# Kernel optimization log

Hardware: AMD Instinct MI355X
Metric: run time of the kernel (lower is better)

## Reference

```python
import jax, jax.numpy as jnp
import numpy as np

EPS = 1e-8  # torch F.cosine_similarity default eps


def _cos_gram(x):
    # row-normalize with eps-clamped norms, then Gram matrix [N, N]
    norms = jnp.maximum(jnp.linalg.norm(x, axis=1, keepdims=True), EPS)
    xn = x / norms
    return xn @ xn.T


def setup_inputs() -> dict:
    key = jax.random.key(0)
    k1, k2 = jax.random.split(key)
    N, D = 8192, 128
    return {
        "feat_q": jax.random.normal(k1, (N, D), dtype=jnp.float32),
        "feat_k": jax.random.normal(k2, (N, D), dtype=jnp.float32),
    }


def reference(feat_q, feat_k):
    feat_k = jax.lax.stop_gradient(feat_k)  # feat_k.detach()
    N = feat_q.shape[0]
    qsim = _cos_gram(feat_q)  # [N, N]
    ksim = _cos_gram(feat_k)  # [N, N]
    # mean of (qsim - ksim)^2 over all off-diagonal (i != j) pairs
    diff2 = (qsim - ksim) ** 2
    off_diag = ~jnp.eye(N, dtype=bool)
    denom = jnp.asarray(N * (N - 1), dtype=diff2.dtype)
    loss = jnp.sum(jnp.where(off_diag, diff2, 0.0)) / denom
    return loss
```

## Files before the change

### kernel.cpp

```cpp
#include <hip/hip_runtime.h>
#include <hip/hip_bf16.h>

#define NROWS 8192
#define DDIM  128
#define KTOT  256
#define GT_ROWB (NROWS * 2)
#define NKCH  32
#define KCH   (NROWS / NKCH)
#define LDSPAD 258

typedef unsigned short ushort_t;
typedef unsigned int   uint_t;
typedef __attribute__((ext_vector_type(8))) short short8;
typedef __attribute__((ext_vector_type(4))) float floatx4;

#define LDS_PTR(p) ((__attribute__((address_space(3))) void*)(p))
#define GLB_PTR(p) ((const __attribute__((address_space(1))) void*)(p))

static __device__ inline ushort_t f2bf(float f) {
    union { float f; uint_t u; } a; a.f = f;
    uint_t u = a.u + 0x7fffu + ((a.u >> 16) & 1u);
    return (ushort_t)(u >> 16);
}

__global__ __launch_bounds__(256) void norm_t_kernel(
    const float* __restrict__ q, const float* __restrict__ k,
    ushort_t* __restrict__ Gt, double* acc)
{
    __shared__ ushort_t lds[64 * LDSPAD];
    if (blockIdx.x == 0 && threadIdx.x == 0) *acc = 0.0;
    int w = threadIdx.x >> 6;
    int l = threadIdx.x & 63;

    #pragma unroll
    for (int i = 0; i < 16; ++i) {
        int rl  = w * 16 + i;
        int row = blockIdx.x * 64 + rl;
        {
            float2 v = ((const float2*)(q + (size_t)row * DDIM))[l];
            float ss = v.x * v.x + v.y * v.y;
            #pragma unroll
            for (int o = 32; o > 0; o >>= 1) ss += __shfl_xor(ss, o, 64);
            float inv = rsqrtf(fmaxf(ss, 1e-16f));
            uint_t p = (uint_t)f2bf(v.x * inv) | ((uint_t)f2bf(v.y * inv) << 16);
            *(uint_t*)&lds[rl * LDSPAD + 2 * l] = p;
        }
        {
            float2 v = ((const float2*)(k + (size_t)row * DDIM))[l];
            float ss = v.x * v.x + v.y * v.y;
            #pragma unroll
            for (int o = 32; o > 0; o >>= 1) ss += __shfl_xor(ss, o, 64);
            float inv = rsqrtf(fmaxf(ss, 1e-16f));
            uint_t p = (uint_t)f2bf(v.x * inv) | ((uint_t)f2bf(v.y * inv) << 16);
            *(uint_t*)&lds[rl * LDSPAD + 128 + 2 * l] = p;
        }
    }
    __syncthreads();

    int a = threadIdx.x;
    char* gdst = (char*)Gt + (size_t)a * GT_ROWB + (size_t)blockIdx.x * 128;
    #pragma unroll
    for (int g = 0; g < 8; ++g) {
        union { ushort_t u16[8]; uint4 v; } tmp;
        #pragma unroll
        for (int e = 0; e < 8; ++e)
            tmp.u16[e] = lds[(g * 8 + e) * LDSPAD + a];
        *(uint4*)(gdst + g * 16) = tmp.v;
    }
}

__global__ __launch_bounds__(128) void gram_a_kernel(
    const ushort_t* __restrict__ Gt, float* __restrict__ P)
{
    __shared__ ushort_t sA[64 * KCH];
    __shared__ ushort_t sB[64 * KCH];

    int tile = blockIdx.x >> 5;
    int c    = blockIdx.x & 31;
    int ti   = tile >> 2, tj = tile & 3;
    int tid  = threadIdx.x;

    const char* gA = (const char*)Gt + (size_t)(ti * 64) * GT_ROWB + c * (KCH * 2);
    const char* gB = (const char*)Gt + (size_t)(tj * 64) * GT_ROWB + c * (KCH * 2);

    #pragma unroll
    for (int it = 0; it < 16; ++it) {
        int chunk = it * 128 + tid;
        int row = chunk >> 5, phys = chunk & 31;
        int logical = phys ^ (row & 7);
        __builtin_amdgcn_global_load_lds(GLB_PTR(gA + (size_t)row * GT_ROWB + logical * 16),
                                         LDS_PTR((char*)sA + chunk * 16), 16, 0, 0);
    }
    #pragma unroll
    for (int it = 0; it < 16; ++it) {
        int chunk = it * 128 + tid;
        int row = chunk >> 5, phys = chunk & 31;
        int logical = phys ^ (row & 7);
        __builtin_amdgcn_global_load_lds(GLB_PTR(gB + (size_t)row * GT_ROWB + logical * 16),
                                         LDS_PTR((char*)sB + chunk * 16), 16, 0, 0);
    }
    __syncthreads();

    int w    = tid >> 6;
    int l    = tid & 63;
    int m    = l & 15;
    int quad = l >> 4;

    floatx4 accC[2][4];
    #pragma unroll
    for (int at = 0; at < 2; ++at)
        #pragma unroll
        for (int bt = 0; bt < 4; ++bt)
            accC[at][bt] = (floatx4){0.f, 0.f, 0.f, 0.f};

    #pragma unroll
    for (int kp = 0; kp < 8; ++kp) {
        short8 af[2], bf[4];
        #pragma unroll
        for (int at = 0; at < 2; ++at) {
            int ra   = w * 32 + at * 16 + m;
            int phys = (kp * 4 + quad) ^ (ra & 7);
            af[at] = *(const short8*)&sA[ra * KCH + phys * 8];
        }
        #pragma unroll
        for (int bt = 0; bt < 4; ++bt) {
            int rb   = bt * 16 + m;
            int phys = (kp * 4 + quad) ^ (rb & 7);
            bf[bt] = *(const short8*)&sB[rb * KCH + phys * 8];
        }
        #pragma unroll
        for (int at = 0; at < 2; ++at)
            #pragma unroll
            for (int bt = 0; bt < 4; ++bt)
                accC[at][bt] = __builtin_amdgcn_mfma_f32_16x16x32_bf16(af[at], bf[bt], accC[at][bt], 0, 0, 0);
    }

    float* pt = P + ((size_t)tile * NKCH + c) * 4096;
    #pragma unroll
    for (int at = 0; at < 2; ++at)
        #pragma unroll
        for (int bt = 0; bt < 4; ++bt)
            #pragma unroll
            for (int r = 0; r < 4; ++r) {
                int row = w * 32 + at * 16 + quad * 4 + r;
                int col = bt * 16 + m;
                pt[row * 64 + col] = accC[at][bt][r];
            }
}

__global__ __launch_bounds__(256) void gram_b_kernel(
    const float* __restrict__ P, double* acc)
{
    __shared__ float wsum[4];
    int e    = blockIdx.x * 256 + threadIdx.x;
    int tile = e >> 12;
    int idx  = e & 4095;

    float s = 0.f;
    #pragma unroll
    for (int c = 0; c < NKCH; ++c)
        s += P[((size_t)tile * NKCH + c) * 4096 + idx];

    int ti = tile >> 2, tj = tile & 3;
    float wgt = ((ti < 2) == (tj < 2)) ? 1.f : -1.f;
    float v = wgt * s * s;

    int w = threadIdx.x >> 6, l = threadIdx.x & 63;
    #pragma unroll
    for (int o = 32; o > 0; o >>= 1) v += __shfl_xor(v, o, 64);
    if (l == 0) wsum[w] = v;
    __syncthreads();
    if (threadIdx.x == 0) {
        double t = (double)wsum[0] + (double)wsum[1] + (double)wsum[2] + (double)wsum[3];
        atomicAdd(acc, t);
    }
}

__global__ void finalize_kernel(const double* acc, float* out) {
    out[0] = (float)(*acc * (1.0 / ((double)NROWS * (double)(NROWS - 1))));
}

extern "C" void kernel_launch(void* const* d_in, const int* in_sizes, int n_in,
                              void* d_out, int out_size, void* d_ws, size_t ws_size,
                              hipStream_t stream) {
    const float* q = (const float*)d_in[0];
    const float* k = (const float*)d_in[1];
    float* out = (float*)d_out;

    double*   acc = (double*)d_ws;
    ushort_t* Gt  = (ushort_t*)((char*)d_ws + 256);
    float*    P   = (float*)((char*)d_ws + 256 + (size_t)KTOT * GT_ROWB);

    norm_t_kernel<<<NROWS / 64, 256, 0, stream>>>(q, k, Gt, acc);
    gram_a_kernel<<<16 * NKCH, 128, 0, stream>>>(Gt, P);
    gram_b_kernel<<<256, 256, 0, stream>>>(P, acc);
    finalize_kernel<<<1, 1, 0, stream>>>(acc, out);
}
```

Baseline: 77.73 us.

## Exploit Gram symmetry, split K finer, vectorize norm loads, fuse finalize

The 256x256 feature Gram over the N dimension is symmetric, so only the 10 upper-triangular 64x64 tile pairs are computed and off-diagonal pairs are weighted by two. The K dimension is split into 64 chunks instead of 32 to raise block count, and gram_a gets a two-block occupancy hint. The normalization kernel uses float4 loads with half-wave row processing and a padded LDS stride. The finalize kernel is removed in favour of a last-block-done atomic counter in gram_b, which saves a launch but adds a fence and an atomic per block.

```diff
diff --git a/kernel.cpp b/kernel.cpp
--- a/kernel.cpp
+++ b/kernel.cpp
@@ -5,9 +5,11 @@
 #define DDIM  128
 #define KTOT  256
 #define GT_ROWB (NROWS * 2)
-#define NKCH  32
-#define KCH   (NROWS / NKCH)
-#define LDSPAD 258
+#define NKCH  64
+#define CHN   (NROWS / NKCH)
+#define NPAIR 10
+#define GB_BLOCKS 160
+#define LDSPAD 260
 
 typedef unsigned short ushort_t;
 typedef unsigned int   uint_t;
@@ -23,36 +25,48 @@
     return (ushort_t)(u >> 16);
 }
 
+static __device__ inline void pair_decode(int p, int* ti, int* tj) {
+    int i = 0, len = 4;
+    while (p >= len) { p -= len; len--; i++; }
+    *ti = i; *tj = i + p;
+}
+
 __global__ __launch_bounds__(256) void norm_t_kernel(
     const float* __restrict__ q, const float* __restrict__ k,
-    ushort_t* __restrict__ Gt, double* acc)
+    ushort_t* __restrict__ Gt, double* acc, uint_t* counter)
 {
     __shared__ ushort_t lds[64 * LDSPAD];
-    if (blockIdx.x == 0 && threadIdx.x == 0) *acc = 0.0;
-    int w = threadIdx.x >> 6;
-    int l = threadIdx.x & 63;
-
-    #pragma unroll
-    for (int i = 0; i < 16; ++i) {
-        int rl  = w * 16 + i;
+    if (blockIdx.x == 0 && threadIdx.x == 0) { *acc = 0.0; *counter = 0u; }
+    int w  = threadIdx.x >> 6;
+    int l  = threadIdx.x & 63;
+    int h  = l >> 5;
+    int li = l & 31;
+
+    #pragma unroll
+    for (int i = 0; i < 8; ++i) {
+        int rl  = w * 16 + 2 * i + h;
         int row = blockIdx.x * 64 + rl;
         {
-            float2 v = ((const float2*)(q + (size_t)row * DDIM))[l];
-            float ss = v.x * v.x + v.y * v.y;
-            #pragma unroll
-            for (int o = 32; o > 0; o >>= 1) ss += __shfl_xor(ss, o, 64);
+            float4 v = ((const float4*)(q + (size_t)row * DDIM))[li];
+            float ss = v.x * v.x + v.y * v.y + v.z * v.z + v.w * v.w;
+            #pragma unroll
+            for (int o = 16; o > 0; o >>= 1) ss += __shfl_xor(ss, o, 64);
             float inv = rsqrtf(fmaxf(ss, 1e-16f));
-            uint_t p = (uint_t)f2bf(v.x * inv) | ((uint_t)f2bf(v.y * inv) << 16);
-            *(uint_t*)&lds[rl * LDSPAD + 2 * l] = p;
+            uint2 p2;
+            p2.x = (uint_t)f2bf(v.x * inv) | ((uint_t)f2bf(v.y * inv) << 16);
+            p2.y = (uint_t)f2bf(v.z * inv) | ((uint_t)f2bf(v.w * inv) << 16);
+            *(uint2*)&lds[rl * LDSPAD + 4 * li] = p2;
         }
         {
-            float2 v = ((const float2*)(k + (size_t)row * DDIM))[l];
-            float ss = v.x * v.x + v.y * v.y;
-            #pragma unroll
-            for (int o = 32; o > 0; o >>= 1) ss += __shfl_xor(ss, o, 64);
+            float4 v = ((const float4*)(k + (size_t)row * DDIM))[li];
+            float ss = v.x * v.x + v.y * v.y + v.z * v.z + v.w * v.w;
+            #pragma unroll
+            for (int o = 16; o > 0; o >>= 1) ss += __shfl_xor(ss, o, 64);
             float inv = rsqrtf(fmaxf(ss, 1e-16f));
-            uint_t p = (uint_t)f2bf(v.x * inv) | ((uint_t)f2bf(v.y * inv) << 16);
-            *(uint_t*)&lds[rl * LDSPAD + 128 + 2 * l] = p;
+            uint2 p2;
+            p2.x = (uint_t)f2bf(v.x * inv) | ((uint_t)f2bf(v.y * inv) << 16);
+            p2.y = (uint_t)f2bf(v.z * inv) | ((uint_t)f2bf(v.w * inv) << 16);
+            *(uint2*)&lds[rl * LDSPAD + 128 + 4 * li] = p2;
         }
     }
     __syncthreads();
@@ -69,35 +83,36 @@
     }
 }
 
-__global__ __launch_bounds__(128) void gram_a_kernel(
+__global__ __launch_bounds__(128, 2) void gram_a_kernel(
     const ushort_t* __restrict__ Gt, float* __restrict__ P)
 {
-    __shared__ ushort_t sA[64 * KCH];
-    __shared__ ushort_t sB[64 * KCH];
-
-    int tile = blockIdx.x >> 5;
-    int c    = blockIdx.x & 31;
-    int ti   = tile >> 2, tj = tile & 3;
-    int tid  = threadIdx.x;
-
-    const char* gA = (const char*)Gt + (size_t)(ti * 64) * GT_ROWB + c * (KCH * 2);
-    const char* gB = (const char*)Gt + (size_t)(tj * 64) * GT_ROWB + c * (KCH * 2);
-
-    #pragma unroll
-    for (int it = 0; it < 16; ++it) {
-        int chunk = it * 128 + tid;
-        int row = chunk >> 5, phys = chunk & 31;
+    __shared__ ushort_t sA[64 * CHN];
+    __shared__ ushort_t sB[64 * CHN];
+
+    int pair = blockIdx.x >> 6;
+    int c    = blockIdx.x & 63;
+    int ti, tj;
+    pair_decode(pair, &ti, &tj);
+    int tid = threadIdx.x;
+
+    const char* gA = (const char*)Gt + (size_t)(ti * 64) * GT_ROWB + c * (CHN * 2);
+    const char* gB = (const char*)Gt + (size_t)(tj * 64) * GT_ROWB + c * (CHN * 2);
+
+    #pragma unroll
+    for (int it = 0; it < 8; ++it) {
+        int ch = it * 128 + tid;
+        int row = ch >> 4, phys = ch & 15;
         int logical = phys ^ (row & 7);
         __builtin_amdgcn_global_load_lds(GLB_PTR(gA + (size_t)row * GT_ROWB + logical * 16),
-                                         LDS_PTR((char*)sA + chunk * 16), 16, 0, 0);
-    }
-    #pragma unroll
-    for (int it = 0; it < 16; ++it) {
-        int chunk = it * 128 + tid;
-        int row = chunk >> 5, phys = chunk & 31;
+                                         LDS_PTR((char*)sA + ch * 16), 16, 0, 0);
+    }
+    #pragma unroll
+    for (int it = 0; it < 8; ++it) {
+        int ch = it * 128 + tid;
+        int row = ch >> 4, phys = ch & 15;
         int logical = phys ^ (row & 7);
         __builtin_amdgcn_global_load_lds(GLB_PTR(gB + (size_t)row * GT_ROWB + logical * 16),
-                                         LDS_PTR((char*)sB + chunk * 16), 16, 0, 0);
+                                         LDS_PTR((char*)sB + ch * 16), 16, 0, 0);
     }
     __syncthreads();
 
@@ -114,19 +129,19 @@
             accC[at][bt] = (floatx4){0.f, 0.f, 0.f, 0.f};
 
     #pragma unroll
-    for (int kp = 0; kp < 8; ++kp) {
+    for (int kp = 0; kp < 4; ++kp) {
         short8 af[2], bf[4];
         #pragma unroll
         for (int at = 0; at < 2; ++at) {
             int ra   = w * 32 + at * 16 + m;
             int phys = (kp * 4 + quad) ^ (ra & 7);
-            af[at] = *(const short8*)&sA[ra * KCH + phys * 8];
+            af[at] = *(const short8*)&sA[ra * CHN + phys * 8];
         }
         #pragma unroll
         for (int bt = 0; bt < 4; ++bt) {
             int rb   = bt * 16 + m;
             int phys = (kp * 4 + quad) ^ (rb & 7);
-            bf[bt] = *(const short8*)&sB[rb * KCH + phys * 8];
+            bf[bt] = *(const short8*)&sB[rb * CHN + phys * 8];
         }
         #pragma unroll
         for (int at = 0; at < 2; ++at)
@@ -135,7 +150,7 @@
                 accC[at][bt] = __builtin_amdgcn_mfma_f32_16x16x32_bf16(af[at], bf[bt], accC[at][bt], 0, 0, 0);
     }
 
-    float* pt = P + ((size_t)tile * NKCH + c) * 4096;
+    float* pt = P + ((size_t)pair * NKCH + c) * 4096;
     #pragma unroll
     for (int at = 0; at < 2; ++at)
         #pragma unroll
@@ -149,20 +164,22 @@
 }
 
 __global__ __launch_bounds__(256) void gram_b_kernel(
-    const float* __restrict__ P, double* acc)
+    const float* __restrict__ P, double* acc, uint_t* counter, float* out)
 {
     __shared__ float wsum[4];
     int e    = blockIdx.x * 256 + threadIdx.x;
-    int tile = e >> 12;
+    int pair = e >> 12;
     int idx  = e & 4095;
 
     float s = 0.f;
     #pragma unroll
     for (int c = 0; c < NKCH; ++c)
-        s += P[((size_t)tile * NKCH + c) * 4096 + idx];
-
-    int ti = tile >> 2, tj = tile & 3;
+        s += P[((size_t)pair * NKCH + c) * 4096 + idx];
+
+    int ti, tj;
+    pair_decode(pair, &ti, &tj);
     float wgt = ((ti < 2) == (tj < 2)) ? 1.f : -1.f;
+    if (ti != tj) wgt *= 2.f;
     float v = wgt * s * s;
 
     int w = threadIdx.x >> 6, l = threadIdx.x & 63;
@@ -173,11 +190,13 @@
     if (threadIdx.x == 0) {
         double t = (double)wsum[0] + (double)wsum[1] + (double)wsum[2] + (double)wsum[3];
         atomicAdd(acc, t);
-    }
-}
-
-__global__ void finalize_kernel(const double* acc, float* out) {
-    out[0] = (float)(*acc * (1.0 / ((double)NROWS * (double)(NROWS - 1))));
+        __threadfence();
+        uint_t old = atomicAdd(counter, 1u);
+        if (old == GB_BLOCKS - 1) {
+            double total = atomicAdd(acc, 0.0);
+            out[0] = (float)(total * (1.0 / ((double)NROWS * (double)(NROWS - 1))));
+        }
+    }
 }
 
 extern "C" void kernel_launch(void* const* d_in, const int* in_sizes, int n_in,
@@ -188,11 +207,11 @@
     float* out = (float*)d_out;
 
     double*   acc = (double*)d_ws;
+    uint_t*   cnt = (uint_t*)((char*)d_ws + 64);
     ushort_t* Gt  = (ushort_t*)((char*)d_ws + 256);
     float*    P   = (float*)((char*)d_ws + 256 + (size_t)KTOT * GT_ROWB);
 
-    norm_t_kernel<<<NROWS / 64, 256, 0, stream>>>(q, k, Gt, acc);
-    gram_a_kernel<<<16 * NKCH, 128, 0, stream>>>(Gt, P);
-    gram_b_kernel<<<256, 256, 0, stream>>>(P, acc);
-    finalize_kernel<<<1, 1, 0, stream>>>(acc, out);
-}
+    norm_t_kernel<<<NROWS / 64, 256, 0, stream>>>(q, k, Gt, acc, cnt);
+    gram_a_kernel<<<NPAIR * NKCH, 128, 0, stream>>>(Gt, P);
+    gram_b_kernel<<<GB_BLOCKS, 256, 0, stream>>>(P, acc, cnt, out);
+}
```

Measured after the change: 76.35 us. About the same (-1.8%).
